# Performance work log

Hardware: AMD Instinct MI355X
Metric: run time of the kernel (lower is better)

Reference implementation:

```python
import jax, jax.numpy as jnp
import numpy as np

B, L, H = 32, 512, 1024
MAX_HEADERS = 32   # static cap on header runs per sample (torch version is dynamic)
MAX_HLEN = 12      # static cap on tokens per header run


def setup_inputs() -> dict:
    key = jax.random.key(0)
    enc = jax.random.normal(key, (B, L, H), dtype=jnp.float32)
    # Structured segments matching the code's semantics: 0=pad, 1=header run,
    # 2=question token (out[s==2]), 3=separator.
    rng = np.random.default_rng(0)
    seg = np.zeros((B, L), dtype=np.int32)
    for b in range(B):
        lq = int(rng.integers(32, 96))
        seg[b, :lq] = 2
        pos = lq
        nh = int(rng.integers(4, MAX_HEADERS))
        for _ in range(nh):
            hl = int(rng.integers(1, MAX_HLEN))
            if pos + hl + 1 >= L:
                break
            seg[b, pos:pos + hl] = 1
            pos += hl
            seg[b, pos] = 3  # separator ends the run
            pos += 1
    return {"encoder_output": enc, "segment": jnp.asarray(seg)}


def _unpack(enc, seg):
    # enc: [B,L,H], seg: [B,L]
    Lloc = enc.shape[1]
    ar = jnp.arange(Lloc)
    # ---- question tokens (seg==2), gathered in order, zero-padded to L ----
    q_mask = seg == 2                                        # [B,L]
    sort_key = jnp.where(q_mask, ar[None, :], Lloc + ar[None, :])
    order = jnp.argsort(sort_key, axis=1)                    # question positions first, in order
    q_gather = jnp.take_along_axis(enc, order[:, :, None], axis=1)
    q_valid = jnp.take_along_axis(q_mask, order, axis=1)
    question_hidden = q_gather * q_valid[:, :, None].astype(enc.dtype)  # [B,L,H]
    # ---- header runs: maximal contiguous stretches of seg==1 ----
    is_h = seg == 1
    prev = jnp.pad(is_h[:, :-1], ((0, 0), (1, 0)))
    run_start = is_h & ~prev                                  # first token of each run
    run_id = jnp.cumsum(run_start.astype(jnp.int32), axis=1) - 1
    last_start = jax.lax.cummax(jnp.where(run_start, ar[None, :], -1), axis=1)
    pos_in_run = ar[None, :] - last_start                     # offset within current run
    valid = is_h & (pos_in_run < MAX_HLEN) & (run_id < MAX_HEADERS)
    hid = jnp.where(valid, run_id, MAX_HEADERS)               # invalid tokens -> dump row
    pid = jnp.clip(pos_in_run, 0, MAX_HLEN - 1)
    buf = jnp.zeros((enc.shape[0], MAX_HEADERS + 1, MAX_HLEN, H), enc.dtype)
    bidx = jnp.arange(enc.shape[0])[:, None]
    buf = buf.at[bidx, hid, pid].set(enc)                     # batched scatter of header tokens
    headers = buf[:, :MAX_HEADERS]                            # [B,MAX_HEADERS,MAX_HLEN,H]
    return question_hidden, headers


def reference(encoder_output, segment):
    return _unpack(encoder_output, segment)
```

## Files before the change

### kernel.cpp

```cpp
#include <hip/hip_runtime.h>

#define BB 32
#define LL 512
#define HH 1024
#define MAXH 32
#define MAXHL 12
#define HROWS (MAXH * MAXHL)
#define RPB 4

#define NQG (LL / RPB)
#define NHG (HROWS / RPB)
#define QBLOCKS (BB * NQG)
#define HBLOCKS (BB * NHG)

__global__ __launch_bounds__(256) void fused_kernel(const float* __restrict__ enc,
                                                    const int* __restrict__ seg,
                                                    float* __restrict__ out) {
    __shared__ int s_src[RPB];
    const int bid = blockIdx.x;
    const int t = threadIdx.x;

    int b, qmode, idx0;
    long long outRow0;
    if (bid < QBLOCKS) {
        b = bid >> 7;
        idx0 = (bid & (NQG - 1)) * RPB;
        qmode = 1;
        outRow0 = (long long)b * LL + idx0;
    } else {
        int hb = bid - QBLOCKS;
        b = hb / NHG;
        idx0 = (hb % NHG) * RPB;
        qmode = 0;
        outRow0 = (long long)BB * LL + (long long)b * HROWS + idx0;
    }

    if (t < 64) {
        if (t < RPB) s_src[t] = -1;
        int s[8];
        const int base = b * LL + t * 8;
#pragma unroll
        for (int k = 0; k < 8; ++k) s[k] = seg[base + k];

        int last_ish = (s[7] == 1) ? 1 : 0;
        int prev_from_left = __shfl_up(last_ish, 1);
        if (t == 0) prev_from_left = 0;

        int qc = 0, rc = 0, mstart = -1;
        {
            int ph = prev_from_left;
#pragma unroll
            for (int k = 0; k < 8; ++k) {
                int ish = (s[k] == 1);
                if (s[k] == 2) qc++;
                if (ish && !ph) { rc++; mstart = t * 8 + k; }
                ph = ish;
            }
        }

        int iq = qc, ir = rc, im = mstart;
#pragma unroll
        for (int off = 1; off < 64; off <<= 1) {
            int uq = __shfl_up(iq, off);
            int ur = __shfl_up(ir, off);
            int um = __shfl_up(im, off);
            if (t >= off) {
                iq += uq;
                ir += ur;
                im = max(im, um);
            }
        }
        int exq = iq - qc;
        int exr = ir - rc;
        int exm = __shfl_up(im, 1);
        if (t == 0) exm = -1;

        {
            int qpos = exq, runs = exr, last = exm, ph = prev_from_left;
#pragma unroll
            for (int k = 0; k < 8; ++k) {
                int i = t * 8 + k;
                int ish = (s[k] == 1);
                if (ish && !ph) { runs++; last = i; }
                if (qmode) {
                    if (s[k] == 2) {
                        int d = qpos - idx0;
                        if (d >= 0 && d < RPB) s_src[d] = i;
                        qpos++;
                    }
                } else if (ish) {
                    int pos = i - last;
                    int rid = runs - 1;
                    if (pos < MAXHL && rid < MAXH) {
                        int d = rid * MAXHL + pos - idx0;
                        if (d >= 0 && d < RPB) s_src[d] = i;
                    }
                }
                ph = ish;
            }
        }
    }
    __syncthreads();

    const long long encBase = (long long)b * LL * HH;
#pragma unroll
    for (int r = 0; r < RPB; ++r) {
        int src = s_src[r];
        float4* dst = reinterpret_cast<float4*>(out + (outRow0 + r) * HH) + t;
        if (src >= 0) {
            const float4* sp = reinterpret_cast<const float4*>(enc + encBase + (long long)src * HH) + t;
            *dst = *sp;
        } else {
            *dst = make_float4(0.f, 0.f, 0.f, 0.f);
        }
    }
}

extern "C" void kernel_launch(void* const* d_in, const int* in_sizes, int n_in,
                              void* d_out, int out_size, void* d_ws, size_t ws_size,
                              hipStream_t stream) {
    const float* enc = (const float*)d_in[0];
    const int* seg = (const int*)d_in[1];
    float* out = (float*)d_out;
    fused_kernel<<<QBLOCKS + HBLOCKS, 256, 0, stream>>>(enc, seg, out);
}
```

Baseline: 25.09 us.

## Have each wavefront compute its own source row and drop shared-memory barrier

Each of the four wavefronts now redundantly scans the segment row and finds its own source index through a wave-wide max reduction, replacing the single-wave scan that wrote to shared memory followed by __syncthreads. Each wave then copies one full row with nontemporal vector loads and stores instead of all 256 threads copying four rows together. This removes the barrier and the idle time of three waves during the scan. In exchange the segment reads and scan work are repeated four times per block, and the nontemporal hints change caching behaviour.

```diff
diff --git a/kernel.cpp b/kernel.cpp
--- a/kernel.cpp
+++ b/kernel.cpp
@@ -13,12 +13,15 @@
 #define QBLOCKS (BB * NQG)
 #define HBLOCKS (BB * NHG)
 
+typedef float f32x4 __attribute__((ext_vector_type(4)));
+
 __global__ __launch_bounds__(256) void fused_kernel(const float* __restrict__ enc,
                                                     const int* __restrict__ seg,
                                                     float* __restrict__ out) {
-    __shared__ int s_src[RPB];
     const int bid = blockIdx.x;
     const int t = threadIdx.x;
+    const int w = t >> 6;
+    const int lane = t & 63;
 
     int b, qmode, idx0;
     long long outRow0;
@@ -34,85 +37,83 @@
         qmode = 0;
         outRow0 = (long long)BB * LL + (long long)b * HROWS + idx0;
     }
+    const int target = idx0 + w;
 
-    if (t < 64) {
-        if (t < RPB) s_src[t] = -1;
-        int s[8];
-        const int base = b * LL + t * 8;
+    int s[8];
+    const int base = b * LL + lane * 8;
 #pragma unroll
-        for (int k = 0; k < 8; ++k) s[k] = seg[base + k];
+    for (int k = 0; k < 8; ++k) s[k] = seg[base + k];
 
-        int last_ish = (s[7] == 1) ? 1 : 0;
-        int prev_from_left = __shfl_up(last_ish, 1);
-        if (t == 0) prev_from_left = 0;
+    int last_ish = (s[7] == 1) ? 1 : 0;
+    int prev_from_left = __shfl_up(last_ish, 1);
+    if (lane == 0) prev_from_left = 0;
 
-        int qc = 0, rc = 0, mstart = -1;
-        {
-            int ph = prev_from_left;
+    int qc = 0, rc = 0, mstart = -1;
+    {
+        int ph = prev_from_left;
 #pragma unroll
-            for (int k = 0; k < 8; ++k) {
-                int ish = (s[k] == 1);
-                if (s[k] == 2) qc++;
-                if (ish && !ph) { rc++; mstart = t * 8 + k; }
-                ph = ish;
-            }
-        }
-
-        int iq = qc, ir = rc, im = mstart;
-#pragma unroll
-        for (int off = 1; off < 64; off <<= 1) {
-            int uq = __shfl_up(iq, off);
-            int ur = __shfl_up(ir, off);
-            int um = __shfl_up(im, off);
-            if (t >= off) {
-                iq += uq;
-                ir += ur;
-                im = max(im, um);
-            }
-        }
-        int exq = iq - qc;
-        int exr = ir - rc;
-        int exm = __shfl_up(im, 1);
-        if (t == 0) exm = -1;
-
-        {
-            int qpos = exq, runs = exr, last = exm, ph = prev_from_left;
-#pragma unroll
-            for (int k = 0; k < 8; ++k) {
-                int i = t * 8 + k;
-                int ish = (s[k] == 1);
-                if (ish && !ph) { runs++; last = i; }
-                if (qmode) {
-                    if (s[k] == 2) {
-                        int d = qpos - idx0;
-                        if (d >= 0 && d < RPB) s_src[d] = i;
-                        qpos++;
-                    }
-                } else if (ish) {
-                    int pos = i - last;
-                    int rid = runs - 1;
-                    if (pos < MAXHL && rid < MAXH) {
-                        int d = rid * MAXHL + pos - idx0;
-                        if (d >= 0 && d < RPB) s_src[d] = i;
-                    }
-                }
-                ph = ish;
-            }
+        for (int k = 0; k < 8; ++k) {
+            int ish = (s[k] == 1);
+            if (s[k] == 2) qc++;
+            if (ish && !ph) { rc++; mstart = lane * 8 + k; }
+            ph = ish;
         }
     }
-    __syncthreads();
 
-    const long long encBase = (long long)b * LL * HH;
+    int iq = qc, ir = rc, im = mstart;
 #pragma unroll
-    for (int r = 0; r < RPB; ++r) {
-        int src = s_src[r];
-        float4* dst = reinterpret_cast<float4*>(out + (outRow0 + r) * HH) + t;
-        if (src >= 0) {
-            const float4* sp = reinterpret_cast<const float4*>(enc + encBase + (long long)src * HH) + t;
-            *dst = *sp;
-        } else {
-            *dst = make_float4(0.f, 0.f, 0.f, 0.f);
+    for (int off = 1; off < 64; off <<= 1) {
+        int uq = __shfl_up(iq, off);
+        int ur = __shfl_up(ir, off);
+        int um = __shfl_up(im, off);
+        if (lane >= off) {
+            iq += uq;
+            ir += ur;
+            im = max(im, um);
         }
+    }
+    int exq = iq - qc;
+    int exr = ir - rc;
+    int exm = __shfl_up(im, 1);
+    if (lane == 0) exm = -1;
+
+    int found = -1;
+    {
+        int qpos = exq, runs = exr, last = exm, ph = prev_from_left;
+#pragma unroll
+        for (int k = 0; k < 8; ++k) {
+            int i = lane * 8 + k;
+            int ish = (s[k] == 1);
+            if (ish && !ph) { runs++; last = i; }
+            if (qmode) {
+                if (s[k] == 2) {
+                    if (qpos == target) found = i;
+                    qpos++;
+                }
+            } else if (ish) {
+                int pos = i - last;
+                int rid = runs - 1;
+                if (pos < MAXHL && rid < MAXH && rid * MAXHL + pos == target) found = i;
+            }
+            ph = ish;
+        }
+    }
+#pragma unroll
+    for (int off = 32; off > 0; off >>= 1) found = max(found, __shfl_xor(found, off));
+
+    f32x4* dst = reinterpret_cast<f32x4*>(out + (outRow0 + w) * HH);
+    if (found >= 0) {
+        const f32x4* sp = reinterpret_cast<const f32x4*>(
+            enc + ((long long)b * LL + found) * HH);
+#pragma unroll
+        for (int j = 0; j < 4; ++j) {
+            f32x4 v = __builtin_nontemporal_load(sp + lane + 64 * j);
+            __builtin_nontemporal_store(v, dst + lane + 64 * j);
+        }
+    } else {
+        f32x4 z = (f32x4)(0.f);
+#pragma unroll
+        for (int j = 0; j < 4; ++j) __builtin_nontemporal_store(z, dst + lane + 64 * j);
     }
 }
 
```

Result: slower. 32.83 us (+30.9%).

## Replace shuffle scans with ballot/popcount and double rows per block

Applied to the files above, without the earlier changes.

Rows per block go from 4 to 8, halving the number of blocks and the redundant per-block segment scans. The shuffle-based prefix scans are replaced with wave ballots plus popcount and clz over strided 64-lane chunks. Each wave now copies its own rows, so the branch on a row's source being present is uniform across the wave. The cost is fewer blocks in flight and more index arithmetic per lane.

```diff
diff --git a/kernel.cpp b/kernel.cpp
--- a/kernel.cpp
+++ b/kernel.cpp
@@ -6,7 +6,7 @@
 #define MAXH 32
 #define MAXHL 12
 #define HROWS (MAXH * MAXHL)
-#define RPB 4
+#define RPB 8
 
 #define NQG (LL / RPB)
 #define NHG (HROWS / RPB)
@@ -23,7 +23,7 @@
     int b, qmode, idx0;
     long long outRow0;
     if (bid < QBLOCKS) {
-        b = bid >> 7;
+        b = bid >> 6;
         idx0 = (bid & (NQG - 1)) * RPB;
         qmode = 1;
         outRow0 = (long long)b * LL + idx0;
@@ -36,82 +36,78 @@
     }
 
     if (t < 64) {
-        if (t < RPB) s_src[t] = -1;
-        int s[8];
-        const int base = b * LL + t * 8;
+        const int lane = t;
+        if (lane < RPB) s_src[lane] = -1;
+
+        int sv[8];
 #pragma unroll
-        for (int k = 0; k < 8; ++k) s[k] = seg[base + k];
+        for (int c = 0; c < 8; ++c) sv[c] = seg[b * LL + c * 64 + lane];
 
-        int last_ish = (s[7] == 1) ? 1 : 0;
-        int prev_from_left = __shfl_up(last_ish, 1);
-        if (t == 0) prev_from_left = 0;
-
-        int qc = 0, rc = 0, mstart = -1;
-        {
-            int ph = prev_from_left;
+        unsigned long long qm[8], hm[8];
 #pragma unroll
-            for (int k = 0; k < 8; ++k) {
-                int ish = (s[k] == 1);
-                if (s[k] == 2) qc++;
-                if (ish && !ph) { rc++; mstart = t * 8 + k; }
-                ph = ish;
-            }
+        for (int c = 0; c < 8; ++c) {
+            qm[c] = __ballot(sv[c] == 2);
+            hm[c] = __ballot(sv[c] == 1);
         }
 
-        int iq = qc, ir = rc, im = mstart;
+        const unsigned long long lm_lt = (1ull << lane) - 1ull;
+        const unsigned long long lm_le = lm_lt | (1ull << lane);
+
+        int qbase = 0;
+        int rbase = 0;
+        int lastrs = -1;
+        int prev_ish = 0;
+
 #pragma unroll
-        for (int off = 1; off < 64; off <<= 1) {
-            int uq = __shfl_up(iq, off);
-            int ur = __shfl_up(ir, off);
-            int um = __shfl_up(im, off);
-            if (t >= off) {
-                iq += uq;
-                ir += ur;
-                im = max(im, um);
-            }
-        }
-        int exq = iq - qc;
-        int exr = ir - rc;
-        int exm = __shfl_up(im, 1);
-        if (t == 0) exm = -1;
+        for (int c = 0; c < 8; ++c) {
+            const unsigned long long rs =
+                hm[c] & ~((hm[c] << 1) | (unsigned long long)prev_ish);
+            const int i = c * 64 + lane;
 
-        {
-            int qpos = exq, runs = exr, last = exm, ph = prev_from_left;
-#pragma unroll
-            for (int k = 0; k < 8; ++k) {
-                int i = t * 8 + k;
-                int ish = (s[k] == 1);
-                if (ish && !ph) { runs++; last = i; }
-                if (qmode) {
-                    if (s[k] == 2) {
-                        int d = qpos - idx0;
-                        if (d >= 0 && d < RPB) s_src[d] = i;
-                        qpos++;
-                    }
-                } else if (ish) {
+            if (qmode) {
+                if (sv[c] == 2) {
+                    int j = qbase + __popcll(qm[c] & lm_lt);
+                    int d = j - idx0;
+                    if (d >= 0 && d < RPB) s_src[d] = i;
+                }
+            } else {
+                if (sv[c] == 1) {
+                    unsigned long long below = rs & lm_le;
+                    int rid = rbase + __popcll(below) - 1;
+                    int last = below ? (c * 64 + 63 - __clzll(below)) : lastrs;
                     int pos = i - last;
-                    int rid = runs - 1;
                     if (pos < MAXHL && rid < MAXH) {
                         int d = rid * MAXHL + pos - idx0;
                         if (d >= 0 && d < RPB) s_src[d] = i;
                     }
                 }
-                ph = ish;
             }
+
+            qbase += __popcll(qm[c]);
+            rbase += __popcll(rs);
+            if (rs) lastrs = c * 64 + 63 - __clzll(rs);
+            prev_ish = (int)(hm[c] >> 63) & 1;
         }
     }
     __syncthreads();
 
+    const int w = t >> 6;
+    const int lane = t & 63;
     const long long encBase = (long long)b * LL * HH;
 #pragma unroll
-    for (int r = 0; r < RPB; ++r) {
-        int src = s_src[r];
-        float4* dst = reinterpret_cast<float4*>(out + (outRow0 + r) * HH) + t;
+    for (int r2 = 0; r2 < RPB / 4; ++r2) {
+        const int r = w * (RPB / 4) + r2;
+        const int src = s_src[r];
+        float4* dst = reinterpret_cast<float4*>(out + (outRow0 + r) * HH);
         if (src >= 0) {
-            const float4* sp = reinterpret_cast<const float4*>(enc + encBase + (long long)src * HH) + t;
-            *dst = *sp;
+            const float4* sp =
+                reinterpret_cast<const float4*>(enc + encBase + (long long)src * HH);
+#pragma unroll
+            for (int j = 0; j < 4; ++j) dst[lane + 64 * j] = sp[lane + 64 * j];
         } else {
-            *dst = make_float4(0.f, 0.f, 0.f, 0.f);
+            const float4 z = make_float4(0.f, 0.f, 0.f, 0.f);
+#pragma unroll
+            for (int j = 0; j < 4; ++j) dst[lane + 64 * j] = z;
         }
     }
 }
```

Result: no change. 24.64 us (-1.8%).
